# Kernel tuning notes

Measured on AMD Instinct MI355X. Metric: run time of the kernel, lower is better.

Reference implementation:

```python
import jax, jax.numpy as jnp
import numpy as np

N_NODES = 50000
N_EDGES = 800000
NODE_DIM = 32
EDGE_DIM = 16
HIDDEN = 64


def setup_inputs() -> dict:
    key = jax.random.key(0)
    ks = jax.random.split(key, 7)
    h = jax.random.normal(ks[0], (N_NODES, HIDDEN), dtype=jnp.float32)
    nf = jax.random.normal(ks[1], (N_NODES, NODE_DIM), dtype=jnp.float32)
    ef = jax.random.normal(ks[2], (N_EDGES, EDGE_DIM), dtype=jnp.float32)
    src = jax.random.randint(ks[3], (N_EDGES,), 0, N_NODES, dtype=jnp.int32)
    dst = jax.random.randint(ks[4], (N_EDGES,), 0, N_NODES, dtype=jnp.int32)
    # torch Linear weights: [out_features, in_features]
    in1 = HIDDEN + 2 * NODE_DIM + EDGE_DIM  # 144
    W1 = jax.random.normal(ks[5], (HIDDEN, in1), dtype=jnp.float32) * (1.0 / np.sqrt(in1))
    W2 = jax.random.normal(ks[6], (HIDDEN, HIDDEN), dtype=jnp.float32) * (1.0 / np.sqrt(HIDDEN))
    return {"h": h, "nf": nf, "ef": ef, "src": src, "dst": dst, "W1": W1, "W2": W2}


def reference(h, nf, ef, src, dst, W1, W2):
    n = nf.shape[0]
    # per-edge message: concat(dst.x, edge.x, src.h)  -> [E, node+edge+hidden]
    m_e = jnp.concatenate([nf[dst], ef, h[src]], axis=-1)
    # mailbox sum per destination node
    m = jax.ops.segment_sum(m_e, dst, num_segments=n)  # [N, node+edge+hidden]
    z = jnp.concatenate([nf, m], axis=-1)              # [N, hidden+2*node+edge]
    new_h = jax.nn.relu(z @ W1.T) @ W2.T               # [N, hidden]
    # DGL update_all only updates nodes that received at least one message
    deg = jax.ops.segment_sum(jnp.ones_like(dst, dtype=jnp.float32), dst, num_segments=n)
    return jnp.where(deg[:, None] > 0, new_h, h)
```

## Files before the change

kernel.cpp:

```cpp
#include <hip/hip_runtime.h>

#define NDIM 32
#define EDIM 16
#define NHID 64
#define NIN1 144
#define SCHUNK 1024
#define SPT 4

__device__ __forceinline__ unsigned pk2(float a, float b) {
  unsigned ua = __float_as_uint(a);
  unsigned ub = __float_as_uint(b);
  ua = (ua + 0x7FFFu + ((ua >> 16) & 1u)) >> 16;
  ub = (ub + 0x7FFFu + ((ub >> 16) & 1u)) >> 16;
  return ua | (ub << 16);
}
__device__ __forceinline__ float lo16(unsigned u) { return __uint_as_float(u << 16); }
__device__ __forceinline__ float hi16(unsigned u) { return __uint_as_float(u & 0xFFFF0000u); }

#define ACC8(A, V)                                   \
  do {                                               \
    A[0] += lo16((V).x); A[1] += hi16((V).x);        \
    A[2] += lo16((V).y); A[3] += hi16((V).y);        \
    A[4] += lo16((V).z); A[5] += hi16((V).z);        \
    A[6] += lo16((V).w); A[7] += hi16((V).w);        \
  } while (0)

__global__ __launch_bounds__(256) void sse_hist(
    const int* __restrict__ dst, int* __restrict__ counts,
    int* __restrict__ rank,
    const float* __restrict__ W1, float* __restrict__ W1T,
    const float* __restrict__ W2, float* __restrict__ W2T,
    const float* __restrict__ h, uint4* __restrict__ h16,
    const float* __restrict__ ef, uint4* __restrict__ ef16,
    int E, int N) {
  int t = blockIdx.x * 256 + threadIdx.x;
  int T = gridDim.x * 256;

  int ebase = blockIdx.x * 1024 + threadIdx.x;
  int r[4];
#pragma unroll
  for (int i = 0; i < 4; ++i) {
    int e = ebase + i * 256;
    if (e < E) r[i] = atomicAdd(&counts[dst[e]], 1);
  }

  if (t < NHID * NIN1) {
    int rr = t / NIN1, k = t - rr * NIN1;
    W1T[k * NHID + rr] = W1[t];
  } else if (t < NHID * NIN1 + NHID * NHID) {
    int i = t - NHID * NIN1;
    int rr = i >> 6, k = i & 63;
    W2T[k * NHID + rr] = W2[i];
  }

  const float4* hf4 = (const float4*)h;
  int NH = N * 8;
  for (int i = t; i < NH; i += T) {
    float4 x = hf4[2 * i], y = hf4[2 * i + 1];
    uint4 o;
    o.x = pk2(x.x, x.y); o.y = pk2(x.z, x.w);
    o.z = pk2(y.x, y.y); o.w = pk2(y.z, y.w);
    h16[i] = o;
  }
  if (ef16) {
    const float4* ef4 = (const float4*)ef;
    int NE = E * 2;
    for (int i = t; i < NE; i += T) {
      float4 x = ef4[2 * i], y = ef4[2 * i + 1];
      uint4 o;
      o.x = pk2(x.x, x.y); o.y = pk2(x.z, x.w);
      o.z = pk2(y.x, y.y); o.w = pk2(y.z, y.w);
      ef16[i] = o;
    }
  }

#pragma unroll
  for (int i = 0; i < 4; ++i) {
    int e = ebase + i * 256;
    if (e < E) rank[e] = r[i];
  }
}

__global__ __launch_bounds__(256) void sse_scan_part(
    const int* __restrict__ counts, int* __restrict__ bsum, int N) {
  __shared__ int ws[4];
  int t = threadIdx.x;
  int base = blockIdx.x * SCHUNK + t * SPT;
  int s = 0;
#pragma unroll
  for (int i = 0; i < SPT; ++i) {
    int idx = base + i;
    if (idx < N) s += counts[idx];
  }
  int v = s;
#pragma unroll
  for (int off = 1; off < 64; off <<= 1) v += __shfl_xor(v, off, 64);
  if ((t & 63) == 0) ws[t >> 6] = v;
  __syncthreads();
  if (t == 0) bsum[blockIdx.x] = ws[0] + ws[1] + ws[2] + ws[3];
}

__global__ __launch_bounds__(256) void sse_scan_final(
    const int* __restrict__ counts, const int* __restrict__ bsum,
    int* __restrict__ starts, int N, int nb) {
  __shared__ int ws[4];
  int t = threadIdx.x;
  int lane = t & 63, w = t >> 6;
  int boff = 0;
  for (int j = 0; j < (int)blockIdx.x; ++j) boff += bsum[j];
  int base = blockIdx.x * SCHUNK + t * SPT;
  int c[SPT];
  int s = 0;
#pragma unroll
  for (int i = 0; i < SPT; ++i) {
    int idx = base + i;
    c[i] = (idx < N) ? counts[idx] : 0;
    s += c[i];
  }
  int incl = s;
#pragma unroll
  for (int off = 1; off < 64; off <<= 1) {
    int u = __shfl_up(incl, off, 64);
    if (lane >= off) incl += u;
  }
  if (lane == 63) ws[w] = incl;
  __syncthreads();
  int woff = 0;
#pragma unroll
  for (int j = 0; j < 4; ++j)
    if (j < w) woff += ws[j];
  int run = boff + woff + (incl - s);
#pragma unroll
  for (int i = 0; i < SPT; ++i) {
    int idx = base + i;
    if (idx < N) {
      starts[idx] = run;
      run += c[i];
    }
  }
  if ((int)blockIdx.x == nb - 1 && t == 0)
    starts[N] = boff + ws[0] + ws[1] + ws[2] + ws[3];
}

__global__ __launch_bounds__(256) void sse_build(
    const int* __restrict__ src, const int* __restrict__ dst,
    const int* __restrict__ rank, const int* __restrict__ starts,
    int2* __restrict__ sedge, int E) {
  int ebase = blockIdx.x * 1024 + threadIdx.x;
#pragma unroll
  for (int i = 0; i < 4; ++i) {
    int e = ebase + i * 256;
    if (e < E) {
      int d = dst[e];
      int pos = starts[d] + rank[e];
      sedge[pos] = make_int2(src[e], e);
    }
  }
}

__global__ __launch_bounds__(256) void sse_gather(
    const uint4* __restrict__ h16, const float* __restrict__ ef,
    const uint4* __restrict__ ef16,
    const int* __restrict__ starts, const int2* __restrict__ sedge,
    uint4* __restrict__ efsum16, uint4* __restrict__ hsum16, int N) {
  int w = threadIdx.x >> 6;
  int lane = threadIdx.x & 63;
  int node = blockIdx.x * 4 + w;
  if (node >= N) return;
  int st = starts[node], en = starts[node + 1];

  int q8 = lane >> 3, m = lane & 7;
  float acc[8];
#pragma unroll
  for (int i = 0; i < 8; ++i) acc[i] = 0.f;

  if (ef16) {
    int eq2 = lane >> 1, em2 = lane & 1;
    float ea8[8];
#pragma unroll
    for (int i = 0; i < 8; ++i) ea8[i] = 0.f;

    for (int base = st; base < en; base += 64) {
      int C = en - base; C = C > 64 ? 64 : C;
      int2 seg = (lane < C) ? sedge[base + lane] : make_int2(0, 0);
      int myS = seg.x, myE = seg.y;
      int nr = (C + 31) >> 5;
      for (int r = 0; r < nr; ++r) {
        int b = r * 32;
        int i0 = b + q8, i1 = b + 8 + q8, i2 = b + 16 + q8, i3 = b + 24 + q8;
        int s0 = __shfl(myS, i0, 64);
        int s1 = __shfl(myS, i1, 64);
        int s2 = __shfl(myS, i2, 64);
        int s3 = __shfl(myS, i3, 64);
        int ie = b + eq2;
        int eid = __shfl(myE, ie, 64);
        uint4 v0 = h16[(size_t)s0 * 8 + m];
        uint4 v1 = h16[(size_t)s1 * 8 + m];
        uint4 v2 = h16[(size_t)s2 * 8 + m];
        uint4 v3 = h16[(size_t)s3 * 8 + m];
        uint4 ev = ef16[(size_t)eid * 2 + em2];
        if (i0 < C) ACC8(acc, v0);
        if (i1 < C) ACC8(acc, v1);
        if (i2 < C) ACC8(acc, v2);
        if (i3 < C) ACC8(acc, v3);
        if (ie < C) ACC8(ea8, ev);
      }
    }
#pragma unroll
    for (int off = 8; off < 64; off <<= 1)
#pragma unroll
      for (int i = 0; i < 8; ++i) acc[i] += __shfl_xor(acc[i], off, 64);
    if (lane < 8) {
      uint4 o;
      o.x = pk2(acc[0], acc[1]); o.y = pk2(acc[2], acc[3]);
      o.z = pk2(acc[4], acc[5]); o.w = pk2(acc[6], acc[7]);
      hsum16[(size_t)node * 8 + lane] = o;
    }
#pragma unroll
    for (int off = 2; off < 64; off <<= 1)
#pragma unroll
      for (int i = 0; i < 8; ++i) ea8[i] += __shfl_xor(ea8[i], off, 64);
    if (lane < 2) {
      uint4 o;
      o.x = pk2(ea8[0], ea8[1]); o.y = pk2(ea8[2], ea8[3]);
      o.z = pk2(ea8[4], ea8[5]); o.w = pk2(ea8[6], ea8[7]);
      efsum16[(size_t)node * 2 + lane] = o;
    }
  } else {
    int eq = lane >> 2, em = lane & 3;
    const float4* ef4 = (const float4*)ef;
    float4 ea = make_float4(0.f, 0.f, 0.f, 0.f);

    for (int base = st; base < en; base += 64) {
      int C = en - base; C = C > 64 ? 64 : C;
      int2 seg = (lane < C) ? sedge[base + lane] : make_int2(0, 0);
      int myS = seg.x, myE = seg.y;
      int nr = (C + 31) >> 5;
      for (int r = 0; r < nr; ++r) {
        int b = r * 32;
        int i0 = b + q8, i1 = b + 8 + q8, i2 = b + 16 + q8, i3 = b + 24 + q8;
        int s0 = __shfl(myS, i0, 64);
        int s1 = __shfl(myS, i1, 64);
        int s2 = __shfl(myS, i2, 64);
        int s3 = __shfl(myS, i3, 64);
        int e0 = b + eq, e1 = b + 16 + eq;
        int id0 = __shfl(myE, e0, 64);
        int id1 = __shfl(myE, e1, 64);
        uint4 v0 = h16[(size_t)s0 * 8 + m];
        uint4 v1 = h16[(size_t)s1 * 8 + m];
        uint4 v2 = h16[(size_t)s2 * 8 + m];
        uint4 v3 = h16[(size_t)s3 * 8 + m];
        float4 x0 = ef4[(size_t)id0 * 4 + em];
        float4 x1 = ef4[(size_t)id1 * 4 + em];
        if (i0 < C) ACC8(acc, v0);
        if (i1 < C) ACC8(acc, v1);
        if (i2 < C) ACC8(acc, v2);
        if (i3 < C) ACC8(acc, v3);
        if (e0 < C) { ea.x += x0.x; ea.y += x0.y; ea.z += x0.z; ea.w += x0.w; }
        if (e1 < C) { ea.x += x1.x; ea.y += x1.y; ea.z += x1.z; ea.w += x1.w; }
      }
    }
#pragma unroll
    for (int off = 8; off < 64; off <<= 1)
#pragma unroll
      for (int i = 0; i < 8; ++i) acc[i] += __shfl_xor(acc[i], off, 64);
    if (lane < 8) {
      uint4 o;
      o.x = pk2(acc[0], acc[1]); o.y = pk2(acc[2], acc[3]);
      o.z = pk2(acc[4], acc[5]); o.w = pk2(acc[6], acc[7]);
      hsum16[(size_t)node * 8 + lane] = o;
    }
#pragma unroll
    for (int off = 4; off < 64; off <<= 1) {
      ea.x += __shfl_xor(ea.x, off, 64);
      ea.y += __shfl_xor(ea.y, off, 64);
      ea.z += __shfl_xor(ea.z, off, 64);
      ea.w += __shfl_xor(ea.w, off, 64);
    }
    float bx = __shfl_xor(ea.x, 1, 64);
    float by = __shfl_xor(ea.y, 1, 64);
    float bz = __shfl_xor(ea.z, 1, 64);
    float bw = __shfl_xor(ea.w, 1, 64);
    if (lane < 4 && (lane & 1) == 0) {
      uint4 o;
      o.x = pk2(ea.x, ea.y); o.y = pk2(ea.z, ea.w);
      o.z = pk2(bx, by);     o.w = pk2(bz, bw);
      efsum16[(size_t)node * 2 + (lane >> 1)] = o;
    }
  }
}

__global__ __launch_bounds__(256) void sse_node(
    const float* __restrict__ h, const float* __restrict__ nf,
    const uint4* __restrict__ efsum16, const uint4* __restrict__ hsum16,
    const int* __restrict__ starts, const float* __restrict__ W1T,
    const float* __restrict__ W2T, float* __restrict__ out, int N) {
  __shared__ float4 zs[36 * 64];
  __shared__ float4 as[16 * 64];

  int tid = threadIdx.x;
  int lane = tid & 63;
  int w = __builtin_amdgcn_readfirstlane(tid) >> 6;

  int node = blockIdx.x * 64 + lane;
  int nodeC = node < N ? node : N - 1;

  if (w == 0) {
    int st = starts[nodeC], en = starts[nodeC + 1];
    float dg = (float)(en - st);
    const float4* nfr = (const float4*)(nf + (size_t)nodeC * NDIM);
#pragma unroll
    for (int k4 = 0; k4 < 8; ++k4) {
      float4 v = nfr[k4];
      zs[k4 * 64 + lane] = v;
      zs[(8 + k4) * 64 + lane] =
          make_float4(dg * v.x, dg * v.y, dg * v.z, dg * v.w);
    }
  } else if (w == 1) {
    uint4 a = efsum16[(size_t)nodeC * 2 + 0];
    uint4 b = efsum16[(size_t)nodeC * 2 + 1];
    zs[16 * 64 + lane] = make_float4(lo16(a.x), hi16(a.x), lo16(a.y), hi16(a.y));
    zs[17 * 64 + lane] = make_float4(lo16(a.z), hi16(a.z), lo16(a.w), hi16(a.w));
    zs[18 * 64 + lane] = make_float4(lo16(b.x), hi16(b.x), lo16(b.y), hi16(b.y));
    zs[19 * 64 + lane] = make_float4(lo16(b.z), hi16(b.z), lo16(b.w), hi16(b.w));
  } else if (w == 2) {
#pragma unroll
    for (int c = 0; c < 4; ++c) {
      uint4 u = hsum16[(size_t)nodeC * 8 + c];
      zs[(20 + 2 * c) * 64 + lane] =
          make_float4(lo16(u.x), hi16(u.x), lo16(u.y), hi16(u.y));
      zs[(21 + 2 * c) * 64 + lane] =
          make_float4(lo16(u.z), hi16(u.z), lo16(u.w), hi16(u.w));
    }
  } else {
#pragma unroll
    for (int c = 4; c < 8; ++c) {
      uint4 u = hsum16[(size_t)nodeC * 8 + c];
      zs[(20 + 2 * c) * 64 + lane] =
          make_float4(lo16(u.x), hi16(u.x), lo16(u.y), hi16(u.y));
      zs[(21 + 2 * c) * 64 + lane] =
          make_float4(lo16(u.z), hi16(u.z), lo16(u.w), hi16(u.w));
    }
  }
  __syncthreads();

  const float4* w1b = (const float4*)W1T + w * 4;
  float a[16];
#pragma unroll
  for (int j = 0; j < 16; ++j) a[j] = 0.f;

#pragma unroll 2
  for (int k4 = 0; k4 < 36; ++k4) {
    float4 zv = zs[k4 * 64 + lane];
#pragma unroll
    for (int kk = 0; kk < 4; ++kk) {
      int k = k4 * 4 + kk;
      float4 w0 = w1b[k * 16 + 0];
      float4 w1 = w1b[k * 16 + 1];
      float4 w2 = w1b[k * 16 + 2];
      float4 w3 = w1b[k * 16 + 3];
      float zk = kk == 0 ? zv.x : kk == 1 ? zv.y : kk == 2 ? zv.z : zv.w;
      a[0]  = fmaf(w0.x, zk, a[0]);
      a[1]  = fmaf(w0.y, zk, a[1]);
      a[2]  = fmaf(w0.z, zk, a[2]);
      a[3]  = fmaf(w0.w, zk, a[3]);
      a[4]  = fmaf(w1.x, zk, a[4]);
      a[5]  = fmaf(w1.y, zk, a[5]);
      a[6]  = fmaf(w1.z, zk, a[6]);
      a[7]  = fmaf(w1.w, zk, a[7]);
      a[8]  = fmaf(w2.x, zk, a[8]);
      a[9]  = fmaf(w2.y, zk, a[9]);
      a[10] = fmaf(w2.z, zk, a[10]);
      a[11] = fmaf(w2.w, zk, a[11]);
      a[12] = fmaf(w3.x, zk, a[12]);
      a[13] = fmaf(w3.y, zk, a[13]);
      a[14] = fmaf(w3.z, zk, a[14]);
      a[15] = fmaf(w3.w, zk, a[15]);
    }
  }

#pragma unroll
  for (int j4 = 0; j4 < 4; ++j4)
    as[(w * 4 + j4) * 64 + lane] =
        make_float4(fmaxf(a[j4 * 4 + 0], 0.f), fmaxf(a[j4 * 4 + 1], 0.f),
                    fmaxf(a[j4 * 4 + 2], 0.f), fmaxf(a[j4 * 4 + 3], 0.f));
  __syncthreads();

  const float4* w2b = (const float4*)W2T + w * 4;
  float o[16];
#pragma unroll
  for (int j = 0; j < 16; ++j) o[j] = 0.f;

#pragma unroll 2
  for (int kq = 0; kq < 16; ++kq) {
    float4 av = as[kq * 64 + lane];
#pragma unroll
    for (int kk = 0; kk < 4; ++kk) {
      int k = kq * 4 + kk;
      float4 w0 = w2b[k * 16 + 0];
      float4 w1 = w2b[k * 16 + 1];
      float4 w2 = w2b[k * 16 + 2];
      float4 w3 = w2b[k * 16 + 3];
      float ak = kk == 0 ? av.x : kk == 1 ? av.y : kk == 2 ? av.z : av.w;
      o[0]  = fmaf(w0.x, ak, o[0]);
      o[1]  = fmaf(w0.y, ak, o[1]);
      o[2]  = fmaf(w0.z, ak, o[2]);
      o[3]  = fmaf(w0.w, ak, o[3]);
      o[4]  = fmaf(w1.x, ak, o[4]);
      o[5]  = fmaf(w1.y, ak, o[5]);
      o[6]  = fmaf(w1.z, ak, o[6]);
      o[7]  = fmaf(w1.w, ak, o[7]);
      o[8]  = fmaf(w2.x, ak, o[8]);
      o[9]  = fmaf(w2.y, ak, o[9]);
      o[10] = fmaf(w2.z, ak, o[10]);
      o[11] = fmaf(w2.w, ak, o[11]);
      o[12] = fmaf(w3.x, ak, o[12]);
      o[13] = fmaf(w3.y, ak, o[13]);
      o[14] = fmaf(w3.z, ak, o[14]);
      o[15] = fmaf(w3.w, ak, o[15]);
    }
  }

  if (node < N) {
    int st = starts[node], en = starts[node + 1];
    float4* o4 = (float4*)(out + (size_t)node * NHID + w * 16);
    if (en - st == 0) {
      const float4* hr = (const float4*)(h + (size_t)node * NHID + w * 16);
#pragma unroll
      for (int j4 = 0; j4 < 4; ++j4) o4[j4] = hr[j4];
    } else {
#pragma unroll
      for (int j4 = 0; j4 < 4; ++j4)
        o4[j4] = make_float4(o[j4 * 4 + 0], o[j4 * 4 + 1], o[j4 * 4 + 2],
                             o[j4 * 4 + 3]);
    }
  }
}

extern "C" void kernel_launch(void* const* d_in, const int* in_sizes, int n_in,
                              void* d_out, int out_size, void* d_ws, size_t ws_size,
                              hipStream_t stream) {
  const float* h  = (const float*)d_in[0];
  const float* nf = (const float*)d_in[1];
  const float* ef = (const float*)d_in[2];
  const int*   src = (const int*)d_in[3];
  const int*   dst = (const int*)d_in[4];
  const float* W1 = (const float*)d_in[5];
  const float* W2 = (const float*)d_in[6];
  float* out = (float*)d_out;

  int N = in_sizes[0] / NHID;
  int E = in_sizes[3];

  char* p = (char*)d_ws;
  int2* sedge = (int2*)p;                 p += (size_t)E * 8;
  int* counts = (int*)p;                  p += (size_t)N * 4;
  int* starts = (int*)p;                  p += (size_t)(N + 1) * 4;
  int* bsum = (int*)p;                    p += 64 * 4;
  float* W1T = (float*)p;                 p += (size_t)NIN1 * NHID * 4;
  float* W2T = (float*)p;                 p += (size_t)NHID * NHID * 4;
  p = (char*)(((size_t)p + 15) & ~(size_t)15);
  uint4* h16 = (uint4*)p;                 p += (size_t)N * 128;
  uint4* efsum16 = (uint4*)p;             p += (size_t)N * 32;
  uint4* hsum16 = (uint4*)p;              p += (size_t)N * 128;
  int* rank = (int*)hsum16;
  uint4* ef16 = (uint4*)p;
  size_t base_used = (size_t)((char*)p - (char*)d_ws);
  if (base_used + (size_t)E * 32 > ws_size) ef16 = nullptr;

  hipMemsetAsync(counts, 0, (size_t)N * sizeof(int), stream);

  int eblocks4 = (E + 1023) / 1024;
  int nb = (N + SCHUNK - 1) / SCHUNK;

  sse_hist<<<eblocks4, 256, 0, stream>>>(dst, counts, rank, W1, W1T, W2, W2T,
                                         h, h16, ef, ef16, E, N);
  sse_scan_part<<<nb, 256, 0, stream>>>(counts, bsum, N);
  sse_scan_final<<<nb, 256, 0, stream>>>(counts, bsum, starts, N, nb);
  sse_build<<<eblocks4, 256, 0, stream>>>(src, dst, rank, starts, sedge, E);

  int gblocks = (N + 3) / 4;
  sse_gather<<<gblocks, 256, 0, stream>>>(h16, ef, ef16, starts, sedge,
                                          efsum16, hsum16, N);

  int nblocks = (N + 63) / 64;
  sse_node<<<nblocks, 256, 0, stream>>>(h, nf, efsum16, hsum16, starts, W1T,
                                        W2T, out, N);
}
```

Baseline: 255.2 us.

## Scatter bf16 edge features into dst-sorted order during CSR build

```diff
diff --git a/kernel.cpp b/kernel.cpp
--- a/kernel.cpp
+++ b/kernel.cpp
@@ -29,13 +29,16 @@
     const int* __restrict__ dst, int* __restrict__ counts,
     int* __restrict__ rank,
     const float* __restrict__ W1, float* __restrict__ W1T,
-    const float* __restrict__ W2, float* __restrict__ W2T,
-    const float* __restrict__ h, uint4* __restrict__ h16,
-    const float* __restrict__ ef, uint4* __restrict__ ef16,
-    int E, int N) {
+    const float* __restrict__ W2, float* __restrict__ W2T, int E) {
   int t = blockIdx.x * 256 + threadIdx.x;
-  int T = gridDim.x * 256;
-
+  if (t < NHID * NIN1) {
+    int r = t / NIN1, k = t - r * NIN1;
+    W1T[k * NHID + r] = W1[t];
+  } else if (t < NHID * NIN1 + NHID * NHID) {
+    int i = t - NHID * NIN1;
+    int r = i >> 6, k = i & 63;
+    W2T[k * NHID + r] = W2[i];
+  }
   int ebase = blockIdx.x * 1024 + threadIdx.x;
   int r[4];
 #pragma unroll
@@ -43,37 +46,6 @@
     int e = ebase + i * 256;
     if (e < E) r[i] = atomicAdd(&counts[dst[e]], 1);
   }
-
-  if (t < NHID * NIN1) {
-    int rr = t / NIN1, k = t - rr * NIN1;
-    W1T[k * NHID + rr] = W1[t];
-  } else if (t < NHID * NIN1 + NHID * NHID) {
-    int i = t - NHID * NIN1;
-    int rr = i >> 6, k = i & 63;
-    W2T[k * NHID + rr] = W2[i];
-  }
-
-  const float4* hf4 = (const float4*)h;
-  int NH = N * 8;
-  for (int i = t; i < NH; i += T) {
-    float4 x = hf4[2 * i], y = hf4[2 * i + 1];
-    uint4 o;
-    o.x = pk2(x.x, x.y); o.y = pk2(x.z, x.w);
-    o.z = pk2(y.x, y.y); o.w = pk2(y.z, y.w);
-    h16[i] = o;
-  }
-  if (ef16) {
-    const float4* ef4 = (const float4*)ef;
-    int NE = E * 2;
-    for (int i = t; i < NE; i += T) {
-      float4 x = ef4[2 * i], y = ef4[2 * i + 1];
-      uint4 o;
-      o.x = pk2(x.x, x.y); o.y = pk2(x.z, x.w);
-      o.z = pk2(y.x, y.y); o.w = pk2(y.z, y.w);
-      ef16[i] = o;
-    }
-  }
-
 #pragma unroll
   for (int i = 0; i < 4; ++i) {
     int e = ebase + i * 256;
@@ -145,23 +117,49 @@
 __global__ __launch_bounds__(256) void sse_build(
     const int* __restrict__ src, const int* __restrict__ dst,
     const int* __restrict__ rank, const int* __restrict__ starts,
-    int2* __restrict__ sedge, int E) {
+    const float* __restrict__ ef, int* __restrict__ ssrc,
+    uint4* __restrict__ sef16,
+    const float* __restrict__ h, uint4* __restrict__ h16,
+    int E, int N) {
   int ebase = blockIdx.x * 1024 + threadIdx.x;
+  const float4* ef4 = (const float4*)ef;
 #pragma unroll
   for (int i = 0; i < 4; ++i) {
     int e = ebase + i * 256;
     if (e < E) {
       int d = dst[e];
       int pos = starts[d] + rank[e];
-      sedge[pos] = make_int2(src[e], e);
-    }
+      ssrc[pos] = src[e];
+      float4 x = ef4[(size_t)e * 4 + 0];
+      float4 y = ef4[(size_t)e * 4 + 1];
+      float4 zq = ef4[(size_t)e * 4 + 2];
+      float4 wq = ef4[(size_t)e * 4 + 3];
+      uint4 o0, o1;
+      o0.x = pk2(x.x, x.y);  o0.y = pk2(x.z, x.w);
+      o0.z = pk2(y.x, y.y);  o0.w = pk2(y.z, y.w);
+      o1.x = pk2(zq.x, zq.y); o1.y = pk2(zq.z, zq.w);
+      o1.z = pk2(wq.x, wq.y); o1.w = pk2(wq.z, wq.w);
+      sef16[(size_t)pos * 2 + 0] = o0;
+      sef16[(size_t)pos * 2 + 1] = o1;
+    }
+  }
+  int t = blockIdx.x * 256 + threadIdx.x;
+  int T = gridDim.x * 256;
+  const float4* hf4 = (const float4*)h;
+  int NH = N * 8;
+  for (int i = t; i < NH; i += T) {
+    float4 x = hf4[2 * i], y = hf4[2 * i + 1];
+    uint4 o;
+    o.x = pk2(x.x, x.y); o.y = pk2(x.z, x.w);
+    o.z = pk2(y.x, y.y); o.w = pk2(y.z, y.w);
+    h16[i] = o;
   }
 }
 
 __global__ __launch_bounds__(256) void sse_gather(
-    const uint4* __restrict__ h16, const float* __restrict__ ef,
-    const uint4* __restrict__ ef16,
-    const int* __restrict__ starts, const int2* __restrict__ sedge,
+    const uint4* __restrict__ h16, const int* __restrict__ ssrc,
+    const uint4* __restrict__ sef16,
+    const int* __restrict__ starts,
     uint4* __restrict__ efsum16, uint4* __restrict__ hsum16, int N) {
   int w = threadIdx.x >> 6;
   int lane = threadIdx.x & 63;
@@ -170,123 +168,57 @@
   int st = starts[node], en = starts[node + 1];
 
   int q8 = lane >> 3, m = lane & 7;
-  float acc[8];
-#pragma unroll
-  for (int i = 0; i < 8; ++i) acc[i] = 0.f;
-
-  if (ef16) {
-    int eq2 = lane >> 1, em2 = lane & 1;
-    float ea8[8];
-#pragma unroll
-    for (int i = 0; i < 8; ++i) ea8[i] = 0.f;
-
-    for (int base = st; base < en; base += 64) {
-      int C = en - base; C = C > 64 ? 64 : C;
-      int2 seg = (lane < C) ? sedge[base + lane] : make_int2(0, 0);
-      int myS = seg.x, myE = seg.y;
-      int nr = (C + 31) >> 5;
-      for (int r = 0; r < nr; ++r) {
-        int b = r * 32;
-        int i0 = b + q8, i1 = b + 8 + q8, i2 = b + 16 + q8, i3 = b + 24 + q8;
-        int s0 = __shfl(myS, i0, 64);
-        int s1 = __shfl(myS, i1, 64);
-        int s2 = __shfl(myS, i2, 64);
-        int s3 = __shfl(myS, i3, 64);
-        int ie = b + eq2;
-        int eid = __shfl(myE, ie, 64);
-        uint4 v0 = h16[(size_t)s0 * 8 + m];
-        uint4 v1 = h16[(size_t)s1 * 8 + m];
-        uint4 v2 = h16[(size_t)s2 * 8 + m];
-        uint4 v3 = h16[(size_t)s3 * 8 + m];
-        uint4 ev = ef16[(size_t)eid * 2 + em2];
-        if (i0 < C) ACC8(acc, v0);
-        if (i1 < C) ACC8(acc, v1);
-        if (i2 < C) ACC8(acc, v2);
-        if (i3 < C) ACC8(acc, v3);
-        if (ie < C) ACC8(ea8, ev);
+  int eh = lane >> 1;
+  float acc[8], ea8[8];
+#pragma unroll
+  for (int i = 0; i < 8; ++i) { acc[i] = 0.f; ea8[i] = 0.f; }
+
+  for (int base = st; base < en; base += 64) {
+    int C = en - base; C = C > 64 ? 64 : C;
+    int myS = (lane < C) ? ssrc[base + lane] : 0;
+    int nr = (C + 31) >> 5;
+    for (int r = 0; r < nr; ++r) {
+      int b = r * 32;
+      int i0 = b + q8, i1 = b + 8 + q8, i2 = b + 16 + q8, i3 = b + 24 + q8;
+      int s0 = __shfl(myS, i0, 64);
+      int s1 = __shfl(myS, i1, 64);
+      int s2 = __shfl(myS, i2, 64);
+      int s3 = __shfl(myS, i3, 64);
+      int ie = b + eh;
+      uint4 v0 = h16[(size_t)s0 * 8 + m];
+      uint4 v1 = h16[(size_t)s1 * 8 + m];
+      uint4 v2 = h16[(size_t)s2 * 8 + m];
+      uint4 v3 = h16[(size_t)s3 * 8 + m];
+      if (ie < C) {
+        uint4 ev = sef16[((size_t)(base + b)) * 2 + lane];
+        ACC8(ea8, ev);
       }
-    }
-#pragma unroll
-    for (int off = 8; off < 64; off <<= 1)
-#pragma unroll
-      for (int i = 0; i < 8; ++i) acc[i] += __shfl_xor(acc[i], off, 64);
-    if (lane < 8) {
-      uint4 o;
-      o.x = pk2(acc[0], acc[1]); o.y = pk2(acc[2], acc[3]);
-      o.z = pk2(acc[4], acc[5]); o.w = pk2(acc[6], acc[7]);
-      hsum16[(size_t)node * 8 + lane] = o;
-    }
-#pragma unroll
-    for (int off = 2; off < 64; off <<= 1)
-#pragma unroll
-      for (int i = 0; i < 8; ++i) ea8[i] += __shfl_xor(ea8[i], off, 64);
-    if (lane < 2) {
-      uint4 o;
-      o.x = pk2(ea8[0], ea8[1]); o.y = pk2(ea8[2], ea8[3]);
-      o.z = pk2(ea8[4], ea8[5]); o.w = pk2(ea8[6], ea8[7]);
-      efsum16[(size_t)node * 2 + lane] = o;
-    }
-  } else {
-    int eq = lane >> 2, em = lane & 3;
-    const float4* ef4 = (const float4*)ef;
-    float4 ea = make_float4(0.f, 0.f, 0.f, 0.f);
-
-    for (int base = st; base < en; base += 64) {
-      int C = en - base; C = C > 64 ? 64 : C;
-      int2 seg = (lane < C) ? sedge[base + lane] : make_int2(0, 0);
-      int myS = seg.x, myE = seg.y;
-      int nr = (C + 31) >> 5;
-      for (int r = 0; r < nr; ++r) {
-        int b = r * 32;
-        int i0 = b + q8, i1 = b + 8 + q8, i2 = b + 16 + q8, i3 = b + 24 + q8;
-        int s0 = __shfl(myS, i0, 64);
-        int s1 = __shfl(myS, i1, 64);
-        int s2 = __shfl(myS, i2, 64);
-        int s3 = __shfl(myS, i3, 64);
-        int e0 = b + eq, e1 = b + 16 + eq;
-        int id0 = __shfl(myE, e0, 64);
-        int id1 = __shfl(myE, e1, 64);
-        uint4 v0 = h16[(size_t)s0 * 8 + m];
-        uint4 v1 = h16[(size_t)s1 * 8 + m];
-        uint4 v2 = h16[(size_t)s2 * 8 + m];
-        uint4 v3 = h16[(size_t)s3 * 8 + m];
-        float4 x0 = ef4[(size_t)id0 * 4 + em];
-        float4 x1 = ef4[(size_t)id1 * 4 + em];
-        if (i0 < C) ACC8(acc, v0);
-        if (i1 < C) ACC8(acc, v1);
-        if (i2 < C) ACC8(acc, v2);
-        if (i3 < C) ACC8(acc, v3);
-        if (e0 < C) { ea.x += x0.x; ea.y += x0.y; ea.z += x0.z; ea.w += x0.w; }
-        if (e1 < C) { ea.x += x1.x; ea.y += x1.y; ea.z += x1.z; ea.w += x1.w; }
-      }
-    }
-#pragma unroll
-    for (int off = 8; off < 64; off <<= 1)
-#pragma unroll
-      for (int i = 0; i < 8; ++i) acc[i] += __shfl_xor(acc[i], off, 64);
-    if (lane < 8) {
-      uint4 o;
-      o.x = pk2(acc[0], acc[1]); o.y = pk2(acc[2], acc[3]);
-      o.z = pk2(acc[4], acc[5]); o.w = pk2(acc[6], acc[7]);
-      hsum16[(size_t)node * 8 + lane] = o;
-    }
-#pragma unroll
-    for (int off = 4; off < 64; off <<= 1) {
-      ea.x += __shfl_xor(ea.x, off, 64);
-      ea.y += __shfl_xor(ea.y, off, 64);
-      ea.z += __shfl_xor(ea.z, off, 64);
-      ea.w += __shfl_xor(ea.w, off, 64);
-    }
-    float bx = __shfl_xor(ea.x, 1, 64);
-    float by = __shfl_xor(ea.y, 1, 64);
-    float bz = __shfl_xor(ea.z, 1, 64);
-    float bw = __shfl_xor(ea.w, 1, 64);
-    if (lane < 4 && (lane & 1) == 0) {
-      uint4 o;
-      o.x = pk2(ea.x, ea.y); o.y = pk2(ea.z, ea.w);
-      o.z = pk2(bx, by);     o.w = pk2(bz, bw);
-      efsum16[(size_t)node * 2 + (lane >> 1)] = o;
-    }
+      if (i0 < C) ACC8(acc, v0);
+      if (i1 < C) ACC8(acc, v1);
+      if (i2 < C) ACC8(acc, v2);
+      if (i3 < C) ACC8(acc, v3);
+    }
+  }
+
+#pragma unroll
+  for (int off = 8; off < 64; off <<= 1)
+#pragma unroll
+    for (int i = 0; i < 8; ++i) acc[i] += __shfl_xor(acc[i], off, 64);
+  if (lane < 8) {
+    uint4 o;
+    o.x = pk2(acc[0], acc[1]); o.y = pk2(acc[2], acc[3]);
+    o.z = pk2(acc[4], acc[5]); o.w = pk2(acc[6], acc[7]);
+    hsum16[(size_t)node * 8 + lane] = o;
+  }
+#pragma unroll
+  for (int off = 2; off < 64; off <<= 1)
+#pragma unroll
+    for (int i = 0; i < 8; ++i) ea8[i] += __shfl_xor(ea8[i], off, 64);
+  if (lane < 2) {
+    uint4 o;
+    o.x = pk2(ea8[0], ea8[1]); o.y = pk2(ea8[2], ea8[3]);
+    o.z = pk2(ea8[4], ea8[5]); o.w = pk2(ea8[6], ea8[7]);
+    efsum16[(size_t)node * 2 + lane] = o;
   }
 }
 
@@ -453,7 +385,8 @@
   int E = in_sizes[3];
 
   char* p = (char*)d_ws;
-  int2* sedge = (int2*)p;                 p += (size_t)E * 8;
+  int* ssrc = (int*)p;                    p += (size_t)E * 4;
+  uint4* sef16 = (uint4*)p;               p += (size_t)E * 32;
   int* counts = (int*)p;                  p += (size_t)N * 4;
   int* starts = (int*)p;                  p += (size_t)(N + 1) * 4;
   int* bsum = (int*)p;                    p += 64 * 4;
@@ -464,23 +397,20 @@
   uint4* efsum16 = (uint4*)p;             p += (size_t)N * 32;
   uint4* hsum16 = (uint4*)p;              p += (size_t)N * 128;
   int* rank = (int*)hsum16;
-  uint4* ef16 = (uint4*)p;
-  size_t base_used = (size_t)((char*)p - (char*)d_ws);
-  if (base_used + (size_t)E * 32 > ws_size) ef16 = nullptr;
 
   hipMemsetAsync(counts, 0, (size_t)N * sizeof(int), stream);
 
   int eblocks4 = (E + 1023) / 1024;
   int nb = (N + SCHUNK - 1) / SCHUNK;
 
-  sse_hist<<<eblocks4, 256, 0, stream>>>(dst, counts, rank, W1, W1T, W2, W2T,
-                                         h, h16, ef, ef16, E, N);
+  sse_hist<<<eblocks4, 256, 0, stream>>>(dst, counts, rank, W1, W1T, W2, W2T, E);
   sse_scan_part<<<nb, 256, 0, stream>>>(counts, bsum, N);
   sse_scan_final<<<nb, 256, 0, stream>>>(counts, bsum, starts, N, nb);
-  sse_build<<<eblocks4, 256, 0, stream>>>(src, dst, rank, starts, sedge, E);
+  sse_build<<<eblocks4, 256, 0, stream>>>(src, dst, rank, starts, ef, ssrc,
+                                          sef16, h, h16, E, N);
 
   int gblocks = (N + 3) / 4;
-  sse_gather<<<gblocks, 256, 0, stream>>>(h16, ef, ef16, starts, sedge,
+  sse_gather<<<gblocks, 256, 0, stream>>>(h16, ssrc, sef16, starts,
                                           efsum16, hsum16, N);
 
   int nblocks = (N + 63) / 64;
```

Measured after the change: 265.6 us. +4.1%, slower.
